# Kernel tuning notes

Hardware: AMD Instinct MI355X
Metric: run time of the kernel (lower is better)

## Reference

```python
import jax, jax.numpy as jnp
import numpy as np

N, F, H, E, G, C = 100000, 128, 128, 640000, 512, 6
EPS = 1e-5


def setup_inputs() -> dict:
    key = jax.random.key(0)
    ks = jax.random.split(key, 20)
    def w(k, shape, fan_in):
        return jax.random.normal(k, shape, jnp.float32) * (1.0 / np.sqrt(fan_in))
    return {
        "x": jax.random.normal(ks[0], (N, F), jnp.float32),
        "edge_index": jax.random.randint(ks[1], (2, E), 0, N),
        "batch": jnp.sort(jax.random.randint(ks[2], (N,), 0, G)),
        "num_graphs": G,
        # SAGEConv1: lin_l (aggregated, with bias) + lin_r (root, no bias)
        "W1l": w(ks[3], (F, H), F), "b1l": jnp.zeros((H,), jnp.float32), "W1r": w(ks[4], (F, H), F),
        # SAGEConv2
        "W2l": w(ks[5], (H, H), H), "b2l": jnp.zeros((H,), jnp.float32), "W2r": w(ks[6], (H, H), H),
        # cluster heads
        "Wc1": w(ks[7], (H, H), H), "bc1": jnp.zeros((H,), jnp.float32),
        "Wc2": w(ks[8], (H, 2), H), "bc2": jnp.zeros((2,), jnp.float32),
        # classifier
        "Wl1": w(ks[9], (H, H), H), "bl1": jnp.zeros((H,), jnp.float32),
        "Wl2": w(ks[10], (H, C), H), "bl2": jnp.zeros((C,), jnp.float32),
    }


def _sage(x, src, dst, Wl, bl, Wr):
    # PyG SAGEConv: mean-aggregate messages x[src] at dst, then lin_l(agg) + lin_r(x)
    n = x.shape[0]
    s = jax.ops.segment_sum(x[src], dst, num_segments=n)
    cnt = jax.ops.segment_sum(jnp.ones((src.shape[0],), x.dtype), dst, num_segments=n)
    agg = s / jnp.maximum(cnt, 1.0)[:, None]
    return agg @ Wl + bl + x @ Wr


def reference(x, edge_index, batch, num_graphs,
              W1l, b1l, W1r, W2l, b2l, W2r,
              Wc1, bc1, Wc2, bc2, Wl1, bl1, Wl2, bl2):
    src, dst = edge_index[0], edge_index[1]
    h = jax.nn.relu(_sage(x, src, dst, W1l, b1l, W1r))
    h = jax.nn.relu(_sage(h, src, dst, W2l, b2l, W2r))
    # 2-way soft cluster assignment per node
    a = jax.nn.softmax(jnp.tanh(h @ Wc1 + bc1) @ Wc2 + bc2, axis=1)  # [N,2]
    g = num_graphs
    # group_features[g] = a_g^T h_g  -> per-node outer product, segment-summed by graph
    gf = jax.ops.segment_sum(a[:, :, None] * h[:, None, :], batch, num_segments=g)  # [G,2,H]
    pos = gf[:, 0, :]  # positive-cluster embedding per graph
    # new_adj[g] = a_g^T A_g a_g ; only within-graph edges appear in the per-graph adj block
    same = (batch[src] == batch[dst]).astype(h.dtype)
    contrib = same[:, None, None] * (a[src][:, :, None] * a[dst][:, None, :])  # [E,2,2]
    new_adj = jax.ops.segment_sum(contrib, batch[src], num_segments=g)  # [G,2,2]
    # F.normalize(p=1, dim=1, eps=1e-5): row-wise L1 with clamped denominator
    l1 = jnp.sum(jnp.abs(new_adj), axis=2, keepdims=True)
    norm_adj = new_adj / jnp.maximum(l1, EPS)
    diag = jnp.diagonal(norm_adj, axis1=1, axis2=2)  # [G,2]
    penalty = jnp.mean(jnp.mean((diag - 1.0) ** 2, axis=1))  # mse vs ones(2), averaged over graphs
    # NOTE: original (faithfully reproduced) takes the mean over ALL nodes, same for every graph
    graph_emb = jnp.broadcast_to(jnp.mean(h, axis=0, keepdims=True), (g, h.shape[1]))
    z = jax.nn.relu(pos @ Wl1 + bl1)  # dropout off (eval mode)
    logits = z @ Wl2 + bl2
    return (jax.nn.log_softmax(logits, axis=-1), pos, graph_emb, penalty)
```

## Files before the change

kernel.cpp:

```cpp
#include <hip/hip_runtime.h>

#define NN 100000
#define NE 640000
#define HD 128
#define NG 512
#define NC 6
#define EPSV 1e-5f

typedef __bf16 bf16_t;
typedef bf16_t bf16x8 __attribute__((ext_vector_type(8)));
typedef float f32x4 __attribute__((ext_vector_type(4)));

__device__ __forceinline__ float b2f(unsigned int u16) {
    return __builtin_bit_cast(float, u16 << 16);
}
__device__ __forceinline__ unsigned short f2b(float f) {
    unsigned int u = __builtin_bit_cast(unsigned int, f);
    unsigned int r = (u + 0x7fffu + ((u >> 16) & 1u)) >> 16;
    return (unsigned short)r;
}

__global__ __launch_bounds__(256) void k_cvt(const float* __restrict__ in,
                                             unsigned short* __restrict__ out, int n8) {
    int i = blockIdx.x * 256 + threadIdx.x;
    if (i >= n8) return;
    float4 v0 = reinterpret_cast<const float4*>(in)[i * 2];
    float4 v1 = reinterpret_cast<const float4*>(in)[i * 2 + 1];
    unsigned short u[8] = {f2b(v0.x), f2b(v0.y), f2b(v0.z), f2b(v0.w),
                           f2b(v1.x), f2b(v1.y), f2b(v1.z), f2b(v1.w)};
    reinterpret_cast<uint4*>(out)[i] = *reinterpret_cast<uint4*>(u);
}

__global__ __launch_bounds__(256) void k_prepw_all(
    const float* __restrict__ Wa, const float* __restrict__ Wb,
    const float* __restrict__ Wc, const float* __restrict__ Wd,
    const float* __restrict__ We, unsigned short* __restrict__ Wt) {
    int i = blockIdx.x * 256 + threadIdx.x;
    int w = i >> 14, r = i & 16383;
    int k = r >> 7, n = r & 127;
    const float* W = (w == 0) ? Wa : (w == 1) ? Wb : (w == 2) ? Wc : (w == 3) ? Wd : We;
    Wt[w * 16384 + n * HD + k] = f2b(W[k * HD + n]);
}

__global__ void k_count(const int* __restrict__ dst, int* __restrict__ cnt) {
    int e = blockIdx.x * blockDim.x + threadIdx.x;
    if (e < NE) atomicAdd(&cnt[dst[e]], 1);
}

__global__ void k_scan1(const int* __restrict__ cnt, int* __restrict__ excl,
                        int* __restrict__ bsum, int n) {
    __shared__ int sh[256];
    int i = blockIdx.x * 256 + threadIdx.x;
    int v = (i < n) ? cnt[i] : 0;
    sh[threadIdx.x] = v;
    __syncthreads();
    for (int off = 1; off < 256; off <<= 1) {
        int t = (threadIdx.x >= off) ? sh[threadIdx.x - off] : 0;
        __syncthreads();
        sh[threadIdx.x] += t;
        __syncthreads();
    }
    if (i < n) excl[i] = sh[threadIdx.x] - v;
    if (threadIdx.x == 255) bsum[blockIdx.x] = sh[255];
}

__global__ void k_scan2(int* bsum, int nb) {
    __shared__ int sh[512];
    int t = threadIdx.x;
    sh[t] = (t < nb) ? bsum[t] : 0;
    __syncthreads();
    for (int off = 1; off < 512; off <<= 1) {
        int v = (t >= off) ? sh[t - off] : 0;
        __syncthreads();
        sh[t] += v;
        __syncthreads();
    }
    if (t < nb) bsum[t] = sh[t];
}

__global__ void k_scan3(const int* __restrict__ excl, const int* __restrict__ bsum,
                        int* __restrict__ row_off, int n) {
    int i = blockIdx.x * 256 + threadIdx.x;
    if (i < n) row_off[i] = excl[i] + (blockIdx.x ? bsum[blockIdx.x - 1] : 0);
    if (i == 0) row_off[n] = NE;
}

__global__ void k_fill(const int* __restrict__ src, const int* __restrict__ dst,
                       const int* __restrict__ row_off, int* __restrict__ cnt,
                       int* __restrict__ csr) {
    int e = blockIdx.x * blockDim.x + threadIdx.x;
    if (e < NE) {
        int d = dst[e];
        int p = atomicSub(&cnt[d], 1);
        __builtin_nontemporal_store(src[e], &csr[row_off[d] + p - 1]);
    }
}

__global__ __launch_bounds__(256) void k_gather_b(const unsigned short* __restrict__ X,
                                                  const int* __restrict__ row_off,
                                                  const int* __restrict__ csr,
                                                  unsigned short* __restrict__ out) {
    int node = (blockIdx.x * blockDim.x + threadIdx.x) >> 6;
    int lane = threadIdx.x & 63;
    if (node >= NN) return;
    int beg = row_off[node], end = row_off[node + 1];
    int grp = lane >> 4;
    int sub = lane & 15;
    float accA[8] = {0.f, 0.f, 0.f, 0.f, 0.f, 0.f, 0.f, 0.f};
    float accB[8] = {0.f, 0.f, 0.f, 0.f, 0.f, 0.f, 0.f, 0.f};
    for (int j = beg; j < end; j += 8) {
        int jj0 = j + grp, jj1 = j + 4 + grp;
        bool ok0 = jj0 < end, ok1 = jj1 < end;
        int s0 = csr[ok0 ? jj0 : beg];
        int s1 = csr[ok1 ? jj1 : beg];
        uint4 v0 = *reinterpret_cast<const uint4*>(X + (size_t)s0 * HD + sub * 8);
        uint4 v1 = *reinterpret_cast<const uint4*>(X + (size_t)s1 * HD + sub * 8);
        if (ok0) {
            accA[0] += b2f(v0.x & 0xffffu); accA[1] += b2f(v0.x >> 16);
            accA[2] += b2f(v0.y & 0xffffu); accA[3] += b2f(v0.y >> 16);
            accA[4] += b2f(v0.z & 0xffffu); accA[5] += b2f(v0.z >> 16);
            accA[6] += b2f(v0.w & 0xffffu); accA[7] += b2f(v0.w >> 16);
        }
        if (ok1) {
            accB[0] += b2f(v1.x & 0xffffu); accB[1] += b2f(v1.x >> 16);
            accB[2] += b2f(v1.y & 0xffffu); accB[3] += b2f(v1.y >> 16);
            accB[4] += b2f(v1.z & 0xffffu); accB[5] += b2f(v1.z >> 16);
            accB[6] += b2f(v1.w & 0xffffu); accB[7] += b2f(v1.w >> 16);
        }
    }
#pragma unroll
    for (int k = 0; k < 8; ++k) {
        float a = accA[k] + accB[k];
        a += __shfl_xor(a, 16, 64);
        a += __shfl_xor(a, 32, 64);
        accA[k] = a;
    }
    if (grp == 0) {
        float inv = 1.f / fmaxf((float)(end - beg), 1.f);
        unsigned short u[8];
#pragma unroll
        for (int k = 0; k < 8; ++k) u[k] = f2b(accA[k] * inv);
        *reinterpret_cast<uint4*>(out + (size_t)node * HD + sub * 8) = *reinterpret_cast<uint4*>(u);
    }
}

__global__ __launch_bounds__(256) void mfma_dual(
    const unsigned short* __restrict__ A1, const unsigned short* __restrict__ W1t,
    const unsigned short* __restrict__ A2, const unsigned short* __restrict__ W2t,
    const float* __restrict__ bias, unsigned short* __restrict__ out, int M)
{
    __shared__ uint4 wlds[2048];
    const int wid = threadIdx.x >> 6;
    const int lane = threadIdx.x & 63;
    const int lrow = lane & 15;
    const int lkg = lane >> 4;
    const int r0 = blockIdx.x * 128 + wid * 32;

    bf16x8 a[2][2][4];
#pragma unroll
    for (int s = 0; s < 2; ++s) {
        const unsigned short* Ap = s ? A2 : A1;
#pragma unroll
        for (int g = 0; g < 2; ++g) {
            int row = r0 + g * 16 + lrow;
            row = row < M ? row : M - 1;
            const unsigned short* p = Ap + (size_t)row * HD + lkg * 8;
#pragma unroll
            for (int ks = 0; ks < 4; ++ks)
                a[s][g][ks] = *reinterpret_cast<const bf16x8*>(p + ks * 32);
        }
    }

    f32x4 acc[2][8];
#pragma unroll
    for (int t = 0; t < 8; ++t) {
        float b = bias[t * 16 + lrow];
        acc[0][t] = (f32x4){b, b, b, b};
        acc[1][t] = (f32x4){b, b, b, b};
    }

    const char* ldsb = (const char*)wlds;
#pragma unroll
    for (int s = 0; s < 2; ++s) {
        const uint4* g4 = reinterpret_cast<const uint4*>(s ? W2t : W1t);
        if (s) __syncthreads();
        for (int i = threadIdx.x; i < 2048; i += 256) {
            int di = i ^ ((i >> 4) & 7);
            wlds[di] = g4[i];
        }
        __syncthreads();
#pragma unroll
        for (int ks = 0; ks < 4; ++ks) {
#pragma unroll
            for (int t = 0; t < 8; ++t) {
                int off = (lrow * 256 + lkg * 16 + t * 4096 + ks * 64) ^ ((lrow & 7) << 4);
                bf16x8 b = *reinterpret_cast<const bf16x8*>(ldsb + off);
                acc[0][t] = __builtin_amdgcn_mfma_f32_16x16x32_bf16(a[s][0][ks], b, acc[0][t], 0, 0, 0);
                acc[1][t] = __builtin_amdgcn_mfma_f32_16x16x32_bf16(a[s][1][ks], b, acc[1][t], 0, 0, 0);
            }
        }
    }

#pragma unroll
    for (int g = 0; g < 2; ++g)
#pragma unroll
        for (int t = 0; t < 8; ++t)
#pragma unroll
            for (int r = 0; r < 4; ++r) {
                int row = r0 + g * 16 + lkg * 4 + r;
                if (row < M) {
                    float v = fmaxf(acc[g][t][r], 0.f);
                    out[(size_t)row * HD + t * 16 + lrow] = f2b(v);
                }
            }
}

__global__ __launch_bounds__(256) void mfma_attn(
    const unsigned short* __restrict__ A1, const unsigned short* __restrict__ W1t,
    const float* __restrict__ bias, const float* __restrict__ Wc2,
    const float* __restrict__ bc2, float* __restrict__ a2, int M)
{
    __shared__ uint4 wlds[2048];
    const int wid = threadIdx.x >> 6;
    const int lane = threadIdx.x & 63;
    const int lrow = lane & 15;
    const int lkg = lane >> 4;
    const int r0 = blockIdx.x * 128 + wid * 32;

    bf16x8 a[2][4];
#pragma unroll
    for (int g = 0; g < 2; ++g) {
        int row = r0 + g * 16 + lrow;
        row = row < M ? row : M - 1;
        const unsigned short* p = A1 + (size_t)row * HD + lkg * 8;
#pragma unroll
        for (int ks = 0; ks < 4; ++ks)
            a[g][ks] = *reinterpret_cast<const bf16x8*>(p + ks * 32);
    }

    f32x4 acc[2][8];
#pragma unroll
    for (int t = 0; t < 8; ++t) {
        float b = bias[t * 16 + lrow];
        acc[0][t] = (f32x4){b, b, b, b};
        acc[1][t] = (f32x4){b, b, b, b};
    }

    const uint4* g4 = reinterpret_cast<const uint4*>(W1t);
    for (int i = threadIdx.x; i < 2048; i += 256) {
        int di = i ^ ((i >> 4) & 7);
        wlds[di] = g4[i];
    }
    __syncthreads();

    const char* ldsb = (const char*)wlds;
#pragma unroll
    for (int ks = 0; ks < 4; ++ks) {
#pragma unroll
        for (int t = 0; t < 8; ++t) {
            int off = (lrow * 256 + lkg * 16 + t * 4096 + ks * 64) ^ ((lrow & 7) << 4);
            bf16x8 b = *reinterpret_cast<const bf16x8*>(ldsb + off);
            acc[0][t] = __builtin_amdgcn_mfma_f32_16x16x32_bf16(a[0][ks], b, acc[0][t], 0, 0, 0);
            acc[1][t] = __builtin_amdgcn_mfma_f32_16x16x32_bf16(a[1][ks], b, acc[1][t], 0, 0, 0);
        }
    }

    float p0[2][4] = {{0.f, 0.f, 0.f, 0.f}, {0.f, 0.f, 0.f, 0.f}};
    float p1[2][4] = {{0.f, 0.f, 0.f, 0.f}, {0.f, 0.f, 0.f, 0.f}};
#pragma unroll
    for (int t = 0; t < 8; ++t) {
        float2 wv = reinterpret_cast<const float2*>(Wc2)[t * 16 + lrow];
#pragma unroll
        for (int g = 0; g < 2; ++g)
#pragma unroll
            for (int r = 0; r < 4; ++r) {
                float tv = tanhf(acc[g][t][r]);
                p0[g][r] = fmaf(tv, wv.x, p0[g][r]);
                p1[g][r] = fmaf(tv, wv.y, p1[g][r]);
            }
    }
#pragma unroll
    for (int off = 1; off < 16; off <<= 1) {
#pragma unroll
        for (int g = 0; g < 2; ++g)
#pragma unroll
            for (int r = 0; r < 4; ++r) {
                p0[g][r] += __shfl_xor(p0[g][r], off, 64);
                p1[g][r] += __shfl_xor(p1[g][r], off, 64);
            }
    }
    if (lrow == 0) {
        float B0 = bc2[0], B1 = bc2[1];
#pragma unroll
        for (int g = 0; g < 2; ++g)
#pragma unroll
            for (int r = 0; r < 4; ++r) {
                int row = r0 + g * 16 + lkg * 4 + r;
                if (row < M) {
                    float u0 = p0[g][r] + B0, u1 = p1[g][r] + B1;
                    float m = fmaxf(u0, u1);
                    float e0 = expf(u0 - m), e1 = expf(u1 - m);
                    float inv = 1.f / (e0 + e1);
                    reinterpret_cast<float2*>(a2)[row] = (float2){e0 * inv, e1 * inv};
                }
            }
    }
}

__global__ __launch_bounds__(512) void k_pos(const unsigned short* __restrict__ h,
                                             const float* __restrict__ a2,
                                             const int* __restrict__ batch,
                                             float* __restrict__ pos_out,
                                             float* __restrict__ csum) {
    __shared__ float4 sh[8][64];
    int g = blockIdx.x;
    int lo = 0, hi = NN;
    while (lo < hi) { int m = (lo + hi) >> 1; if (batch[m] < g) lo = m + 1; else hi = m; }
    int beg = lo;
    hi = NN;
    while (lo < hi) { int m = (lo + hi) >> 1; if (batch[m] < g + 1) lo = m + 1; else hi = m; }
    int end = lo;
    int grp = threadIdx.x >> 6;
    int lane = threadIdx.x & 63;
    float4 acc = {0.f, 0.f, 0.f, 0.f};
    for (int i = beg + grp; i < end; i += 8) {
        float a = a2[i * 2];
        unsigned int v = *reinterpret_cast<const unsigned int*>(h + (size_t)i * HD + lane * 2);
        float f0 = b2f(v & 0xffffu), f1 = b2f(v >> 16);
        acc.x = fmaf(a, f0, acc.x);
        acc.y = fmaf(a, f1, acc.y);
        acc.z += f0;
        acc.w += f1;
    }
    sh[grp][lane] = acc;
    __syncthreads();
    if (threadIdx.x < 64) {
        float4 s = sh[0][lane];
#pragma unroll
        for (int k = 1; k < 8; ++k) {
            float4 t = sh[k][lane];
            s.x += t.x; s.y += t.y; s.z += t.z; s.w += t.w;
        }
        reinterpret_cast<float2*>(pos_out)[g * 64 + lane] = (float2){s.x, s.y};
        atomicAdd(&csum[lane * 2], s.z);
        atomicAdd(&csum[lane * 2 + 1], s.w);
    }
}

__global__ void k_gemb(const float* __restrict__ csum, float* __restrict__ out) {
    int i = blockIdx.x * 256 + threadIdx.x;
    out[i] = csum[i & 127] * (1.f / (float)NN);
}

__global__ __launch_bounds__(256) void k_adj(const int* __restrict__ src, const int* __restrict__ dst,
                                             const int* __restrict__ batch, const float* __restrict__ a2,
                                             float* __restrict__ adj) {
    __shared__ float sh[NG * 4];
    for (int i = threadIdx.x; i < NG * 4; i += 256) sh[i] = 0.f;
    __syncthreads();
    for (int e = blockIdx.x * 256 + threadIdx.x; e < NE; e += gridDim.x * 256) {
        int s = src[e], d = dst[e];
        int bs = batch[s], bd = batch[d];
        if (bs != bd) continue;
        float a0s = a2[2 * s], a1s = a2[2 * s + 1];
        float a0d = a2[2 * d], a1d = a2[2 * d + 1];
        float* A = sh + bs * 4;
        atomicAdd(A + 0, a0s * a0d);
        atomicAdd(A + 1, a0s * a1d);
        atomicAdd(A + 2, a1s * a0d);
        atomicAdd(A + 3, a1s * a1d);
    }
    __syncthreads();
    for (int i = threadIdx.x; i < NG * 4; i += 256) {
        float v = sh[i];
        if (v != 0.f) atomicAdd(&adj[i], v);
    }
}

__global__ void k_penalty(const float* __restrict__ adj, float* __restrict__ out) {
    __shared__ float sh[512];
    int g = threadIdx.x;
    float x0 = adj[g * 4], x1 = adj[g * 4 + 1], x2 = adj[g * 4 + 2], x3 = adj[g * 4 + 3];
    float l0 = fabsf(x0) + fabsf(x1);
    float l1 = fabsf(x2) + fabsf(x3);
    float d0 = x0 / fmaxf(l0, EPSV);
    float d1 = x3 / fmaxf(l1, EPSV);
    sh[g] = 0.5f * ((d0 - 1.f) * (d0 - 1.f) + (d1 - 1.f) * (d1 - 1.f));
    __syncthreads();
    for (int off = 256; off >= 1; off >>= 1) {
        if (g < off) sh[g] += sh[g + off];
        __syncthreads();
    }
    if (g == 0) out[0] = sh[0] * (1.f / (float)NG);
}

__global__ __launch_bounds__(256) void gemm_head(
    const float* __restrict__ A, const float* __restrict__ W,
    const float* __restrict__ bias, float* __restrict__ out, int M)
{
    const int tid = threadIdx.x;
    const int w = __builtin_amdgcn_readfirstlane(tid >> 6);
    const int lane = tid & 63;
    const int r0 = blockIdx.x * 32 + w * 8;
    if (r0 >= M) return;
    const int c0 = lane, c1 = lane + 64;
    float acc0[8], acc1[8];
    const float b0 = bias[c0], b1 = bias[c1];
#pragma unroll
    for (int r = 0; r < 8; ++r) { acc0[r] = b0; acc1[r] = b1; }
    const float* Ap = A + (size_t)r0 * HD;
    for (int k4 = 0; k4 < HD / 4; ++k4) {
        float4 a[8];
#pragma unroll
        for (int r = 0; r < 8; ++r)
            a[r] = *reinterpret_cast<const float4*>(Ap + r * HD + k4 * 4);
#pragma unroll
        for (int j = 0; j < 4; ++j) {
            const int k = k4 * 4 + j;
            const float w0 = W[k * HD + c0];
            const float w1 = W[k * HD + c1];
#pragma unroll
            for (int r = 0; r < 8; ++r) {
                const float av = (j == 0) ? a[r].x : (j == 1) ? a[r].y
                               : (j == 2) ? a[r].z : a[r].w;
                acc0[r] = fmaf(av, w0, acc0[r]);
                acc1[r] = fmaf(av, w1, acc1[r]);
            }
        }
    }
#pragma unroll
    for (int r = 0; r < 8; ++r) {
        out[(size_t)(r0 + r) * HD + c0] = fmaxf(acc0[r], 0.f);
        out[(size_t)(r0 + r) * HD + c1] = fmaxf(acc1[r], 0.f);
    }
}

__global__ void k_head(const float* __restrict__ z, const float* __restrict__ Wl2,
                       const float* __restrict__ bl2, float* __restrict__ out0) {
    int g = blockIdx.x * blockDim.x + threadIdx.x;
    if (g >= NG) return;
    float l[NC];
#pragma unroll
    for (int c = 0; c < NC; ++c) l[c] = bl2[c];
    for (int k = 0; k < HD; ++k) {
        float zv = z[(size_t)g * HD + k];
#pragma unroll
        for (int c = 0; c < NC; ++c) l[c] = fmaf(zv, Wl2[k * NC + c], l[c]);
    }
    float m = l[0];
#pragma unroll
    for (int c = 1; c < NC; ++c) m = fmaxf(m, l[c]);
    float sum = 0.f;
#pragma unroll
    for (int c = 0; c < NC; ++c) sum += expf(l[c] - m);
    float lse = m + logf(sum);
#pragma unroll
    for (int c = 0; c < NC; ++c) out0[g * NC + c] = l[c] - lse;
}

extern "C" void kernel_launch(void* const* d_in, const int* in_sizes, int n_in,
                              void* d_out, int out_size, void* d_ws, size_t ws_size,
                              hipStream_t stream) {
    const float* x   = (const float*)d_in[0];
    const int*   ei  = (const int*)d_in[1];
    const int*   src = ei;
    const int*   dst = ei + NE;
    const int*   batch = (const int*)d_in[2];
    const float* W1l = (const float*)d_in[4];
    const float* b1l = (const float*)d_in[5];
    const float* W1r = (const float*)d_in[6];
    const float* W2l = (const float*)d_in[7];
    const float* b2l = (const float*)d_in[8];
    const float* W2r = (const float*)d_in[9];
    const float* Wc1 = (const float*)d_in[10];
    const float* bc1 = (const float*)d_in[11];
    const float* Wc2 = (const float*)d_in[12];
    const float* bc2 = (const float*)d_in[13];
    const float* Wl1 = (const float*)d_in[14];
    const float* bl1 = (const float*)d_in[15];
    const float* Wl2 = (const float*)d_in[16];
    const float* bl2 = (const float*)d_in[17];

    char* ws = (char*)d_ws;
    const size_t BB = (size_t)NN * HD * 2;
    unsigned short* xb   = (unsigned short*)(ws);
    unsigned short* bufA = (unsigned short*)(ws + BB);
    unsigned short* bufB = (unsigned short*)(ws + 2 * BB);
    size_t O = 3 * BB;
    int*   cnt     = (int*)(ws + O);
    float* adj     = (float*)(ws + O + 400000);
    float* csum    = (float*)(ws + O + 408192);
    int*   excl    = (int*)(ws + O + 408704);
    int*   row_off = (int*)(ws + O + 808704);
    int*   csr     = (int*)(ws + O + 1208768);
    int*   bsum    = (int*)(ws + O + 3768768);
    float* a2      = (float*)(ws + O + 3772864);
    float* zbuf    = (float*)(ws + O + 4572864);
    unsigned short* w1lt = (unsigned short*)(ws + O + 4835008);
    unsigned short* w1rt = w1lt + 16384;
    unsigned short* w2lt = w1rt + 16384;
    unsigned short* w2rt = w2lt + 16384;
    unsigned short* wc1t = w2rt + 16384;

    float* out0 = (float*)d_out;
    float* pos  = out0 + NG * NC;
    float* gemb = pos + NG * HD;
    float* pen  = gemb + NG * HD;

    hipMemsetAsync(ws + O, 0, 408704, stream);

    k_cvt<<<6250, 256, 0, stream>>>(x, xb, NN * HD / 8);
    k_prepw_all<<<320, 256, 0, stream>>>(W1l, W1r, W2l, W2r, Wc1, w1lt);

    k_count<<<NE / 256, 256, 0, stream>>>(dst, cnt);
    k_scan1<<<391, 256, 0, stream>>>(cnt, excl, bsum, NN);
    k_scan2<<<1, 512, 0, stream>>>(bsum, 391);
    k_scan3<<<391, 256, 0, stream>>>(excl, bsum, row_off, NN);
    k_fill<<<NE / 256, 256, 0, stream>>>(src, dst, row_off, cnt, csr);

    const int GEMM_GRID = (NN + 127) / 128;
    k_gather_b<<<NN / 4, 256, 0, stream>>>(xb, row_off, csr, bufA);
    mfma_dual<<<GEMM_GRID, 256, 0, stream>>>(bufA, w1lt, xb, w1rt, b1l, bufB, NN);
    k_gather_b<<<NN / 4, 256, 0, stream>>>(bufB, row_off, csr, bufA);
    mfma_dual<<<GEMM_GRID, 256, 0, stream>>>(bufA, w2lt, bufB, w2rt, b2l, xb, NN);
    mfma_attn<<<GEMM_GRID, 256, 0, stream>>>(xb, wc1t, bc1, Wc2, bc2, a2, NN);
    k_pos<<<NG, 512, 0, stream>>>(xb, a2, batch, pos, csum);
    k_gemb<<<NG * HD / 256, 256, 0, stream>>>(csum, gemb);
    k_adj<<<120, 256, 0, stream>>>(src, dst, batch, a2, adj);
    k_penalty<<<1, 512, 0, stream>>>(adj, pen);
    gemm_head<<<NG / 32, 256, 0, stream>>>(pos, Wl1, bl1, zbuf, NG);
    k_head<<<2, 256, 0, stream>>>(zbuf, Wl2, bl2, out0);
}
```

Before: 336.4 us.

## Fuse preprocessing kernels and partition CSR build by destination range

```diff
diff --git a/kernel.cpp b/kernel.cpp
--- a/kernel.cpp
+++ b/kernel.cpp
@@ -6,6 +6,7 @@
 #define NG 512
 #define NC 6
 #define EPSV 1e-5f
+#define OCT 12500
 
 typedef __bf16 bf16_t;
 typedef bf16_t bf16x8 __attribute__((ext_vector_type(8)));
@@ -20,79 +21,79 @@
     return (unsigned short)r;
 }
 
-__global__ __launch_bounds__(256) void k_cvt(const float* __restrict__ in,
-                                             unsigned short* __restrict__ out, int n8) {
-    int i = blockIdx.x * 256 + threadIdx.x;
-    if (i >= n8) return;
-    float4 v0 = reinterpret_cast<const float4*>(in)[i * 2];
-    float4 v1 = reinterpret_cast<const float4*>(in)[i * 2 + 1];
-    unsigned short u[8] = {f2b(v0.x), f2b(v0.y), f2b(v0.z), f2b(v0.w),
-                           f2b(v1.x), f2b(v1.y), f2b(v1.z), f2b(v1.w)};
-    reinterpret_cast<uint4*>(out)[i] = *reinterpret_cast<uint4*>(u);
-}
-
-__global__ __launch_bounds__(256) void k_prepw_all(
+__global__ __launch_bounds__(256) void k_prep(
+    const float* __restrict__ x, unsigned short* __restrict__ xb,
     const float* __restrict__ Wa, const float* __restrict__ Wb,
     const float* __restrict__ Wc, const float* __restrict__ Wd,
-    const float* __restrict__ We, unsigned short* __restrict__ Wt) {
-    int i = blockIdx.x * 256 + threadIdx.x;
-    int w = i >> 14, r = i & 16383;
-    int k = r >> 7, n = r & 127;
-    const float* W = (w == 0) ? Wa : (w == 1) ? Wb : (w == 2) ? Wc : (w == 3) ? Wd : We;
-    Wt[w * 16384 + n * HD + k] = f2b(W[k * HD + n]);
-}
-
-__global__ void k_count(const int* __restrict__ dst, int* __restrict__ cnt) {
-    int e = blockIdx.x * blockDim.x + threadIdx.x;
-    if (e < NE) atomicAdd(&cnt[dst[e]], 1);
-}
-
-__global__ void k_scan1(const int* __restrict__ cnt, int* __restrict__ excl,
-                        int* __restrict__ bsum, int n) {
-    __shared__ int sh[256];
-    int i = blockIdx.x * 256 + threadIdx.x;
-    int v = (i < n) ? cnt[i] : 0;
-    sh[threadIdx.x] = v;
+    const float* __restrict__ We, unsigned short* __restrict__ Wt,
+    const int* __restrict__ dst, int* __restrict__ cnt)
+{
+    int bid = blockIdx.x;
+    if (bid < 6250) {
+        int i = bid * 256 + threadIdx.x;
+        float4 v0 = reinterpret_cast<const float4*>(x)[i * 2];
+        float4 v1 = reinterpret_cast<const float4*>(x)[i * 2 + 1];
+        unsigned short u[8] = {f2b(v0.x), f2b(v0.y), f2b(v0.z), f2b(v0.w),
+                               f2b(v1.x), f2b(v1.y), f2b(v1.z), f2b(v1.w)};
+        reinterpret_cast<uint4*>(xb)[i] = *reinterpret_cast<uint4*>(u);
+    } else if (bid < 6570) {
+        int i = (bid - 6250) * 256 + threadIdx.x;
+        int w = i >> 14, r = i & 16383;
+        int k = r >> 7, n = r & 127;
+        const float* W = (w == 0) ? Wa : (w == 1) ? Wb : (w == 2) ? Wc : (w == 3) ? Wd : We;
+        Wt[w * 16384 + n * HD + k] = f2b(W[k * HD + n]);
+    } else {
+        int q = bid - 6570;
+        int oct = q & 7;
+        int widx = q >> 3;
+        int lo = oct * OCT, hi = lo + OCT;
+        for (int e = widx * 256 + threadIdx.x; e < NE; e += 120 * 256) {
+            int d = dst[e];
+            if (d >= lo && d < hi) atomicAdd(&cnt[d], 1);
+        }
+    }
+}
+
+__global__ __launch_bounds__(1024) void k_scan_one(const int* __restrict__ cnt,
+                                                   int* __restrict__ row_off) {
+    __shared__ int sh[1024];
+    const int CH = 98;
+    int t = threadIdx.x;
+    int beg = t * CH, end = beg + CH;
+    if (end > NN) end = NN;
+    int s = 0;
+    for (int i = beg; i < end; ++i) s += cnt[i];
+    sh[t] = s;
     __syncthreads();
-    for (int off = 1; off < 256; off <<= 1) {
-        int t = (threadIdx.x >= off) ? sh[threadIdx.x - off] : 0;
-        __syncthreads();
-        sh[threadIdx.x] += t;
-        __syncthreads();
-    }
-    if (i < n) excl[i] = sh[threadIdx.x] - v;
-    if (threadIdx.x == 255) bsum[blockIdx.x] = sh[255];
-}
-
-__global__ void k_scan2(int* bsum, int nb) {
-    __shared__ int sh[512];
-    int t = threadIdx.x;
-    sh[t] = (t < nb) ? bsum[t] : 0;
-    __syncthreads();
-    for (int off = 1; off < 512; off <<= 1) {
+    for (int off = 1; off < 1024; off <<= 1) {
         int v = (t >= off) ? sh[t - off] : 0;
         __syncthreads();
         sh[t] += v;
         __syncthreads();
     }
-    if (t < nb) bsum[t] = sh[t];
-}
-
-__global__ void k_scan3(const int* __restrict__ excl, const int* __restrict__ bsum,
-                        int* __restrict__ row_off, int n) {
-    int i = blockIdx.x * 256 + threadIdx.x;
-    if (i < n) row_off[i] = excl[i] + (blockIdx.x ? bsum[blockIdx.x - 1] : 0);
-    if (i == 0) row_off[n] = NE;
-}
-
-__global__ void k_fill(const int* __restrict__ src, const int* __restrict__ dst,
-                       const int* __restrict__ row_off, int* __restrict__ cnt,
-                       int* __restrict__ csr) {
-    int e = blockIdx.x * blockDim.x + threadIdx.x;
-    if (e < NE) {
+    int run = t ? sh[t - 1] : 0;
+    for (int i = beg; i < end; ++i) {
+        row_off[i] = run;
+        run += cnt[i];
+    }
+    if (t == 1023) row_off[NN] = NE;
+}
+
+__global__ __launch_bounds__(256) void k_fill(const int* __restrict__ src,
+                                              const int* __restrict__ dst,
+                                              const int* __restrict__ row_off,
+                                              int* __restrict__ cnt,
+                                              int* __restrict__ csr) {
+    int q = blockIdx.x;
+    int oct = q & 7;
+    int widx = q >> 3;
+    int lo = oct * OCT, hi = lo + OCT;
+    for (int e = widx * 256 + threadIdx.x; e < NE; e += 120 * 256) {
         int d = dst[e];
-        int p = atomicSub(&cnt[d], 1);
-        __builtin_nontemporal_store(src[e], &csr[row_off[d] + p - 1]);
+        if (d >= lo && d < hi) {
+            int p = atomicSub(&cnt[d], 1);
+            csr[row_off[d] + p - 1] = src[e];
+        }
     }
 }
 
@@ -490,13 +491,11 @@
     int*   cnt     = (int*)(ws + O);
     float* adj     = (float*)(ws + O + 400000);
     float* csum    = (float*)(ws + O + 408192);
-    int*   excl    = (int*)(ws + O + 408704);
-    int*   row_off = (int*)(ws + O + 808704);
-    int*   csr     = (int*)(ws + O + 1208768);
-    int*   bsum    = (int*)(ws + O + 3768768);
-    float* a2      = (float*)(ws + O + 3772864);
-    float* zbuf    = (float*)(ws + O + 4572864);
-    unsigned short* w1lt = (unsigned short*)(ws + O + 4835008);
+    int*   row_off = (int*)(ws + O + 408704);
+    int*   csr     = (int*)(ws + O + 808768);
+    float* a2      = (float*)(ws + O + 3368768);
+    float* zbuf    = (float*)(ws + O + 4168768);
+    unsigned short* w1lt = (unsigned short*)(ws + O + 4430912);
     unsigned short* w1rt = w1lt + 16384;
     unsigned short* w2lt = w1rt + 16384;
     unsigned short* w2rt = w2lt + 16384;
@@ -509,14 +508,9 @@
 
     hipMemsetAsync(ws + O, 0, 408704, stream);
 
-    k_cvt<<<6250, 256, 0, stream>>>(x, xb, NN * HD / 8);
-    k_prepw_all<<<320, 256, 0, stream>>>(W1l, W1r, W2l, W2r, Wc1, w1lt);
-
-    k_count<<<NE / 256, 256, 0, stream>>>(dst, cnt);
-    k_scan1<<<391, 256, 0, stream>>>(cnt, excl, bsum, NN);
-    k_scan2<<<1, 512, 0, stream>>>(bsum, 391);
-    k_scan3<<<391, 256, 0, stream>>>(excl, bsum, row_off, NN);
-    k_fill<<<NE / 256, 256, 0, stream>>>(src, dst, row_off, cnt, csr);
+    k_prep<<<7530, 256, 0, stream>>>(x, xb, W1l, W1r, W2l, W2r, Wc1, w1lt, dst, cnt);
+    k_scan_one<<<1, 1024, 0, stream>>>(cnt, row_off);
+    k_fill<<<960, 256, 0, stream>>>(src, dst, row_off, cnt, csr);
 
     const int GEMM_GRID = (NN + 127) / 128;
     k_gather_b<<<NN / 4, 256, 0, stream>>>(xb, row_off, csr, bufA);
```

Measured after the change: 468.4 us. +39.3%, slower.
